# Kernel tuning notes

Hardware: AMD Instinct MI355X
Metric: run time of the kernel (lower is better)

## Reference

```python
import jax, jax.numpy as jnp
import numpy as np

D = 256; H = 8; L = 4; P = 4; DFF = 1024
B = 4; NQ = 900
SHAPES = np.array([[100, 160], [50, 80], [25, 40], [13, 20]], dtype=np.int64)
NV = int((SHAPES[:, 0] * SHAPES[:, 1]).sum())


def setup_inputs():
    key = jax.random.key(0)
    ks = jax.random.split(key, 16)
    def w(k, shape):
        return jax.random.normal(k, shape, jnp.float32) * 0.02
    return {
        "tgt": jax.random.normal(ks[0], (B, NQ, D), jnp.float32),
        "tgt_query_pos": jax.random.normal(ks[1], (B, NQ, D), jnp.float32),
        "tgt_reference_points": jax.random.uniform(ks[2], (B, NQ, L, 2), dtype=jnp.float32),
        "memory": jax.random.normal(ks[3], (B, NV, D), jnp.float32),
        "value_proj_w": w(ks[4], (D, D)), "value_proj_b": jnp.zeros((D,), jnp.float32),
        "samp_off_w": w(ks[5], (H * L * P * 2, D)), "samp_off_b": jnp.zeros((H * L * P * 2,), jnp.float32),
        "attn_w_w": w(ks[6], (H * L * P, D)), "attn_w_b": jnp.zeros((H * L * P,), jnp.float32),
        "ca_out_w": w(ks[7], (D, D)), "ca_out_b": jnp.zeros((D,), jnp.float32),
        "ln1_g": jnp.ones((D,), jnp.float32), "ln1_b": jnp.zeros((D,), jnp.float32),
        "in_proj_w": w(ks[8], (3 * D, D)), "in_proj_b": jnp.zeros((3 * D,), jnp.float32),
        "sa_out_w": w(ks[9], (D, D)), "sa_out_b": jnp.zeros((D,), jnp.float32),
        "ln2_g": jnp.ones((D,), jnp.float32), "ln2_b": jnp.zeros((D,), jnp.float32),
        "ffn1_w": w(ks[10], (DFF, D)), "ffn1_b": jnp.zeros((DFF,), jnp.float32),
        "ffn2_w": w(ks[11], (D, DFF)), "ffn2_b": jnp.zeros((D,), jnp.float32),
        "ln3_g": jnp.ones((D,), jnp.float32), "ln3_b": jnp.zeros((D,), jnp.float32),
        "spatial_shapes": jnp.asarray(SHAPES),
    }


def layer_norm(x, g, b, eps=1e-5):
    m = x.mean(-1, keepdims=True)
    v = ((x - m) ** 2).mean(-1, keepdims=True)
    return (x - m) / jnp.sqrt(v + eps) * g + b


def ms_deform_attn(query, refp, value, shapes, Wv, bv, Wo, bo, Wa, ba, Wout, bout):
    # query [B,Nq,D], refp [B,Nq,L,2] in [0,1], value [B,NV,D]; shapes: np [L,2] (H,W)
    Bq, Nq, Dm = query.shape
    dh = Dm // H
    v = (value @ Wv.T + bv).reshape(Bq, -1, H, dh)
    off = (query @ Wo.T + bo).reshape(Bq, Nq, H, L, P, 2)
    aw = jax.nn.softmax((query @ Wa.T + ba).reshape(Bq, Nq, H, L * P), axis=-1)
    aw = aw.reshape(Bq, Nq, H, L, P)
    norm = jnp.asarray(np.stack([shapes[:, 1], shapes[:, 0]], -1), jnp.float32)  # [L,2] = (W,H)
    loc = refp[:, :, None, :, None, :] + off / norm[None, None, None, :, None, :]  # [B,Nq,H,L,P,2]
    starts = np.concatenate([[0], np.cumsum(shapes[:, 0] * shapes[:, 1])])
    acc = jnp.zeros((Bq, Nq, H, dh), query.dtype)
    for l in range(L):
        Hl, Wl = int(shapes[l, 0]), int(shapes[l, 1])
        vf = v[:, int(starts[l]):int(starts[l]) + Hl * Wl]                 # [B,HW,H,dh]
        v2 = vf.transpose(0, 2, 1, 3).reshape(Bq * H, Hl * Wl, dh)
        # grid_sample align_corners=False: pixel = loc*size - 0.5
        xl = loc[:, :, :, l, :, 0] * Wl - 0.5                              # [B,Nq,H,P]
        yl = loc[:, :, :, l, :, 1] * Hl - 0.5
        x0 = jnp.floor(xl); y0 = jnp.floor(yl)
        wx = xl - x0; wy = yl - y0
        x0i = x0.astype(jnp.int32); y0i = y0.astype(jnp.int32)
        def corner(xi, yi, wgt):
            valid = (xi >= 0) & (xi < Wl) & (yi >= 0) & (yi < Hl)
            idx = jnp.clip(yi, 0, Hl - 1) * Wl + jnp.clip(xi, 0, Wl - 1)   # [B,Nq,H,P]
            idx2 = idx.transpose(0, 2, 1, 3).reshape(Bq * H, Nq * P)
            g = jnp.take_along_axis(v2, idx2[..., None], axis=1)           # [B*H,Nq*P,dh]
            g = g.reshape(Bq, H, Nq, P, dh).transpose(0, 2, 1, 3, 4)
            return g * (wgt * valid).astype(query.dtype)[..., None]
        s = (corner(x0i, y0i, (1 - wx) * (1 - wy))
             + corner(x0i + 1, y0i, wx * (1 - wy))
             + corner(x0i, y0i + 1, (1 - wx) * wy)
             + corner(x0i + 1, y0i + 1, wx * wy))                          # [B,Nq,H,P,dh]
        acc = acc + jnp.einsum('bqhpd,bqhp->bqhd', s, aw[:, :, :, l])
    return acc.reshape(Bq, Nq, Dm) @ Wout.T + bout


def mha(q, k, v, Win, bin_, Wout, bout):
    Dm = q.shape[-1]; dh = Dm // H
    def proj(x, W, b):
        return (x @ W.T + b).reshape(x.shape[0], x.shape[1], H, dh)
    qh = proj(q, Win[:Dm], bin_[:Dm])
    kh = proj(k, Win[Dm:2 * Dm], bin_[Dm:2 * Dm])
    vh = proj(v, Win[2 * Dm:], bin_[2 * Dm:])
    att = jax.nn.softmax(jnp.einsum('bqhd,bkhd->bhqk', qh, kh) / np.sqrt(dh).astype(np.float32), axis=-1)
    o = jnp.einsum('bhqk,bkhd->bqhd', att, vh).reshape(q.shape[0], q.shape[1], Dm)
    return o @ Wout.T + bout


def _forward(tgt, tgt_query_pos, tgt_reference_points, memory,
             value_proj_w, value_proj_b, samp_off_w, samp_off_b, attn_w_w, attn_w_b,
             ca_out_w, ca_out_b, ln1_g, ln1_b, in_proj_w, in_proj_b, sa_out_w, sa_out_b,
             ln2_g, ln2_b, ffn1_w, ffn1_b, ffn2_w, ffn2_b, ln3_g, ln3_b, shapes):
    # cross (deformable) attention
    q = tgt + tgt_query_pos
    tgt2 = ms_deform_attn(q, tgt_reference_points, memory, shapes,
                          value_proj_w, value_proj_b, samp_off_w, samp_off_b,
                          attn_w_w, attn_w_b, ca_out_w, ca_out_b)
    x = layer_norm(tgt + tgt2, ln1_g, ln1_b)
    # self attention (q=k=x+pos, v=x)
    qk = x + tgt_query_pos
    x = layer_norm(x + mha(qk, qk, x, in_proj_w, in_proj_b, sa_out_w, sa_out_b), ln2_g, ln2_b)
    # FFN
    ff = jax.nn.relu(x @ ffn1_w.T + ffn1_b) @ ffn2_w.T + ffn2_b
    return layer_norm(x + ff, ln3_g, ln3_b)


def reference(tgt, tgt_query_pos, tgt_reference_points, memory,
              value_proj_w, value_proj_b, samp_off_w, samp_off_b, attn_w_w, attn_w_b,
              ca_out_w, ca_out_b, ln1_g, ln1_b, in_proj_w, in_proj_b, sa_out_w, sa_out_b,
              ln2_g, ln2_b, ffn1_w, ffn1_b, ffn2_w, ffn2_b, ln3_g, ln3_b, spatial_shapes):
    shapes = np.asarray(spatial_shapes)
    return _forward(tgt, tgt_query_pos, tgt_reference_points, memory,
                    value_proj_w, value_proj_b, samp_off_w, samp_off_b, attn_w_w, attn_w_b,
                    ca_out_w, ca_out_b, ln1_g, ln1_b, in_proj_w, in_proj_b, sa_out_w, sa_out_b,
                    ln2_g, ln2_b, ffn1_w, ffn1_b, ffn2_w, ffn2_b, ln3_g, ln3_b, shapes)
```

## Files before the change

kernel.cpp:

```cpp
#include <hip/hip_runtime.h>

constexpr int D_   = 256;
constexpr int H_   = 8;
constexpr int DH   = 32;
constexpr int L_   = 4;
constexpr int P_   = 4;
constexpr int DFF_ = 1024;
constexpr int B_   = 4;
constexpr int NQ_  = 900;
constexpr int NV_  = 21260;
constexpr int MQ   = B_ * NQ_;
constexpr int MV   = B_ * NV_;

typedef __attribute__((ext_vector_type(8))) short short8;
typedef __attribute__((ext_vector_type(4))) float f32x4;

static __device__ __forceinline__ unsigned short f2bf(float x) {
  union { float f; unsigned int u; } v;
  v.f = x;
  const unsigned int r = v.u + 0x7fffu + ((v.u >> 16) & 1u);
  return (unsigned short)(r >> 16);
}
static __device__ __forceinline__ float bf2f(unsigned short u) {
  union { unsigned int i; float f; } x;
  x.i = ((unsigned int)u) << 16;
  return x.f;
}

struct CvtArgs {
  const float* src[9];
  unsigned short* dst[9];
  int n[9];
  float scl[9];
};

__global__ __launch_bounds__(256) void cvtw(CvtArgs a) {
  const int seg = blockIdx.y;
  const int n = a.n[seg];
  const float s = a.scl[seg];
  const float* __restrict__ sp = a.src[seg];
  unsigned short* __restrict__ d = a.dst[seg];
  for (int i = (blockIdx.x * 256 + threadIdx.x) * 4; i < n;
       i += gridDim.x * 256 * 4) {
    const float4 v = *reinterpret_cast<const float4*>(&sp[i]);
    d[i + 0] = f2bf(v.x * s); d[i + 1] = f2bf(v.y * s);
    d[i + 2] = f2bf(v.z * s); d[i + 3] = f2bf(v.w * s);
  }
}

__global__ void biasprep(const float* __restrict__ bin,
                         const float* __restrict__ bo,
                         const float* __restrict__ ba,
                         float* __restrict__ bqk, float* __restrict__ bfu) {
  const int i = threadIdx.x;
  if (i < 512) bqk[i] = (i < 256) ? bin[i] * 0.17677669529663687f : bin[i];
  if (i < 384) bfu[i] = (i < 256) ? bo[i] : ba[i - 256];
}

template <int K, bool ABF, bool ADD2, bool RELU, bool OUTBF>
__global__ __launch_bounds__(256) void gemm_p2(
    const void* __restrict__ Ap, const float* __restrict__ A2,
    const unsigned short* __restrict__ Wbf, const float* __restrict__ bias,
    void* __restrict__ Cp, int M, int N) {
  constexpr int LDR = 40;
  constexpr int NT = K / 32;
  __shared__ unsigned short As[2][128][LDR];
  __shared__ unsigned short Bs[2][128][LDR];

  const float* Af = (const float*)Ap;
  const unsigned short* Ab = (const unsigned short*)Ap;
  float* Cf = (float*)Cp;
  unsigned short* Cb = (unsigned short*)Cp;

  const int t    = threadIdx.x;
  const int wave = t >> 6;
  const int l    = t & 63;
  const int n0   = blockIdx.x * 128;
  const int m0   = blockIdx.y * 128;
  const int wm   = (wave >> 1) * 64;
  const int wn   = (wave & 1) * 64;
  const int srow = t >> 1;
  const int sseg = (t & 1) * 16;
  const int lr   = l & 15;
  const int lk   = (l >> 4) * 8;

  const int am = m0 + srow;
  const bool aok = am < M;
  const size_t arow = (size_t)am * K;
  const size_t brow = (size_t)(n0 + srow) * K;

  f32x4 acc[4][4];
#pragma unroll
  for (int i = 0; i < 4; ++i)
#pragma unroll
    for (int j = 0; j < 4; ++j) acc[i][j] = (f32x4)0.f;

  float  frA[16], frB[16];
  short8 abA0, abA1, abB0, abB1;
  short8 brA0, brA1, brB0, brB1;

#define LOAD_SLOT(SUF, k0)                                                     \
  do {                                                                         \
    if constexpr (ABF) {                                                       \
      if (aok) {                                                               \
        ab##SUF##0 = *reinterpret_cast<const short8*>(&Ab[arow + (k0) + sseg]);\
        ab##SUF##1 = *reinterpret_cast<const short8*>(&Ab[arow + (k0) + sseg + 8]);\
      } else {                                                                 \
        ab##SUF##0 = (short8)(short)0; ab##SUF##1 = (short8)(short)0;          \
      }                                                                        \
    } else {                                                                   \
      if (aok) {                                                               \
        _Pragma("unroll")                                                      \
        for (int j = 0; j < 4; ++j) {                                          \
          const float4 av =                                                    \
              *reinterpret_cast<const float4*>(&Af[arow + (k0) + sseg + 4 * j]);\
          fr##SUF[4 * j + 0] = av.x; fr##SUF[4 * j + 1] = av.y;                \
          fr##SUF[4 * j + 2] = av.z; fr##SUF[4 * j + 3] = av.w;                \
        }                                                                      \
        if constexpr (ADD2) {                                                  \
          _Pragma("unroll")                                                    \
          for (int j = 0; j < 4; ++j) {                                        \
            const float4 av =                                                  \
                *reinterpret_cast<const float4*>(&A2[arow + (k0) + sseg + 4 * j]);\
            fr##SUF[4 * j + 0] += av.x; fr##SUF[4 * j + 1] += av.y;            \
            fr##SUF[4 * j + 2] += av.z; fr##SUF[4 * j + 3] += av.w;            \
          }                                                                    \
        }                                                                      \
      } else {                                                                 \
        _Pragma("unroll")                                                      \
        for (int j = 0; j < 16; ++j) fr##SUF[j] = 0.f;                         \
      }                                                                        \
    }                                                                          \
    br##SUF##0 = *reinterpret_cast<const short8*>(&Wbf[brow + (k0) + sseg]);   \
    br##SUF##1 = *reinterpret_cast<const short8*>(&Wbf[brow + (k0) + sseg + 8]);\
  } while (0)

#define WRITE_SLOT(SUF, BUF)                                                   \
  do {                                                                         \
    if constexpr (ABF) {                                                       \
      *reinterpret_cast<short8*>(&As[BUF][srow][sseg])     = ab##SUF##0;       \
      *reinterpret_cast<short8*>(&As[BUF][srow][sseg + 8]) = ab##SUF##1;       \
    } else {                                                                   \
      alignas(16) unsigned short u[16];                                        \
      _Pragma("unroll")                                                        \
      for (int j = 0; j < 16; ++j) u[j] = f2bf(fr##SUF[j]);                    \
      *reinterpret_cast<short8*>(&As[BUF][srow][sseg]) =                       \
          *reinterpret_cast<short8*>(&u[0]);                                   \
      *reinterpret_cast<short8*>(&As[BUF][srow][sseg + 8]) =                   \
          *reinterpret_cast<short8*>(&u[8]);                                   \
    }                                                                          \
    *reinterpret_cast<short8*>(&Bs[BUF][srow][sseg])     = br##SUF##0;         \
    *reinterpret_cast<short8*>(&Bs[BUF][srow][sseg + 8]) = br##SUF##1;         \
  } while (0)

#define MFMA_STEP(BUF)                                                         \
  do {                                                                         \
    short8 af0 = *reinterpret_cast<const short8*>(&As[BUF][wm +  0 + lr][lk]); \
    short8 af1 = *reinterpret_cast<const short8*>(&As[BUF][wm + 16 + lr][lk]); \
    short8 af2 = *reinterpret_cast<const short8*>(&As[BUF][wm + 32 + lr][lk]); \
    short8 af3 = *reinterpret_cast<const short8*>(&As[BUF][wm + 48 + lr][lk]); \
    short8 bf0 = *reinterpret_cast<const short8*>(&Bs[BUF][wn +  0 + lr][lk]); \
    short8 bf1 = *reinterpret_cast<const short8*>(&Bs[BUF][wn + 16 + lr][lk]); \
    short8 bf2 = *reinterpret_cast<const short8*>(&Bs[BUF][wn + 32 + lr][lk]); \
    short8 bf3 = *reinterpret_cast<const short8*>(&Bs[BUF][wn + 48 + lr][lk]); \
    acc[0][0] = __builtin_amdgcn_mfma_f32_16x16x32_bf16(af0, bf0, acc[0][0], 0, 0, 0); \
    acc[0][1] = __builtin_amdgcn_mfma_f32_16x16x32_bf16(af0, bf1, acc[0][1], 0, 0, 0); \
    acc[0][2] = __builtin_amdgcn_mfma_f32_16x16x32_bf16(af0, bf2, acc[0][2], 0, 0, 0); \
    acc[0][3] = __builtin_amdgcn_mfma_f32_16x16x32_bf16(af0, bf3, acc[0][3], 0, 0, 0); \
    acc[1][0] = __builtin_amdgcn_mfma_f32_16x16x32_bf16(af1, bf0, acc[1][0], 0, 0, 0); \
    acc[1][1] = __builtin_amdgcn_mfma_f32_16x16x32_bf16(af1, bf1, acc[1][1], 0, 0, 0); \
    acc[1][2] = __builtin_amdgcn_mfma_f32_16x16x32_bf16(af1, bf2, acc[1][2], 0, 0, 0); \
    acc[1][3] = __builtin_amdgcn_mfma_f32_16x16x32_bf16(af1, bf3, acc[1][3], 0, 0, 0); \
    acc[2][0] = __builtin_amdgcn_mfma_f32_16x16x32_bf16(af2, bf0, acc[2][0], 0, 0, 0); \
    acc[2][1] = __builtin_amdgcn_mfma_f32_16x16x32_bf16(af2, bf1, acc[2][1], 0, 0, 0); \
    acc[2][2] = __builtin_amdgcn_mfma_f32_16x16x32_bf16(af2, bf2, acc[2][2], 0, 0, 0); \
    acc[2][3] = __builtin_amdgcn_mfma_f32_16x16x32_bf16(af2, bf3, acc[2][3], 0, 0, 0); \
    acc[3][0] = __builtin_amdgcn_mfma_f32_16x16x32_bf16(af3, bf0, acc[3][0], 0, 0, 0); \
    acc[3][1] = __builtin_amdgcn_mfma_f32_16x16x32_bf16(af3, bf1, acc[3][1], 0, 0, 0); \
    acc[3][2] = __builtin_amdgcn_mfma_f32_16x16x32_bf16(af3, bf2, acc[3][2], 0, 0, 0); \
    acc[3][3] = __builtin_amdgcn_mfma_f32_16x16x32_bf16(af3, bf3, acc[3][3], 0, 0, 0); \
  } while (0)

  LOAD_SLOT(A, 0);
  LOAD_SLOT(B, 32);
#pragma unroll
  for (int tt = 0; tt < NT; tt += 2) {
    WRITE_SLOT(A, 0);
    if (tt + 2 < NT) LOAD_SLOT(A, (tt + 2) * 32);
    __syncthreads();
    MFMA_STEP(0);

    WRITE_SLOT(B, 1);
    if (tt + 3 < NT) LOAD_SLOT(B, (tt + 3) * 32);
    __syncthreads();
    MFMA_STEP(1);
  }
#undef LOAD_SLOT
#undef WRITE_SLOT
#undef MFMA_STEP

  const int orow = (l >> 4) * 4;
#pragma unroll
  for (int fi = 0; fi < 4; ++fi) {
#pragma unroll
    for (int fj = 0; fj < 4; ++fj) {
      const int n = n0 + wn + fj * 16 + lr;
      const float bn = bias[n];
#pragma unroll
      for (int i = 0; i < 4; ++i) {
        const int m = m0 + wm + fi * 16 + orow + i;
        if (m < M) {
          float vv = acc[fi][fj][i] + bn;
          if (RELU) vv = fmaxf(vv, 0.f);
          if (OUTBF)
            Cb[(size_t)m * N + n] = f2bf(vv);
          else
            Cf[(size_t)m * N + n] = vv;
        }
      }
    }
  }
}

template <bool ABF, bool ADD2, bool RELU, bool OUTBF>
__global__ __launch_bounds__(256) void gemm_bres(
    const void* __restrict__ Ap, const float* __restrict__ A2,
    const unsigned short* __restrict__ Wbf, const float* __restrict__ bias,
    void* __restrict__ Cp, int M, int N) {
  __shared__ unsigned short Bs[32768];
  __shared__ unsigned short As[2][64][40];

  const float* Af = (const float*)Ap;
  const unsigned short* Ab = (const unsigned short*)Ap;
  float* Cf = (float*)Cp;
  unsigned short* Cb = (unsigned short*)Cp;

  const int t    = threadIdx.x;
  const int wave = t >> 6;
  const int l    = t & 63;
  const int n0   = blockIdx.x * 128;
  const int m0   = blockIdx.y * 64;
  const int wm   = (wave >> 1) * 32;
  const int wcg  = (wave & 1) * 4;
  const int lr   = l & 15;
  const int lk8  = (l >> 4) * 8;

#pragma unroll
  for (int i = 0; i < 16; ++i) {
    const int e  = i * 256 + t;
    const int el = e & 63;
    const int cg = (e >> 6) & 7;
    const int st = e >> 9;
    const int row = n0 + cg * 16 + (el & 15);
    const int col = st * 32 + ((el >> 4) * 8);
    *reinterpret_cast<short8*>(&Bs[e * 8]) =
        *reinterpret_cast<const short8*>(&Wbf[(size_t)row * 256 + col]);
  }

  const int arow = t >> 2;
  const int acol = (t & 3) * 8;
  const int am   = m0 + arow;
  const bool aok = am < M;
  const size_t abase = (size_t)am * 256 + acol;

  float  fr[3][8];
  short8 br_[3];

  auto ALOAD = [&](int slot, int tt) {
    const int k0 = tt * 32;
    if constexpr (ABF) {
      br_[slot] = aok ? *reinterpret_cast<const short8*>(&Ab[abase + k0])
                      : (short8)(short)0;
    } else {
      if (aok) {
        const float4 a0 = *reinterpret_cast<const float4*>(&Af[abase + k0]);
        const float4 a1 = *reinterpret_cast<const float4*>(&Af[abase + k0 + 4]);
        fr[slot][0] = a0.x; fr[slot][1] = a0.y;
        fr[slot][2] = a0.z; fr[slot][3] = a0.w;
        fr[slot][4] = a1.x; fr[slot][5] = a1.y;
        fr[slot][6] = a1.z; fr[slot][7] = a1.w;
        if constexpr (ADD2) {
          const float4 b0 = *reinterpret_cast<const float4*>(&A2[abase + k0]);
          const float4 b1 = *reinterpret_cast<const float4*>(&A2[abase + k0 + 4]);
          fr[slot][0] += b0.x; fr[slot][1] += b0.y;
          fr[slot][2] += b0.z; fr[slot][3] += b0.w;
          fr[slot][4] += b1.x; fr[slot][5] += b1.y;
          fr[slot][6] += b1.z; fr[slot][7] += b1.w;
        }
      } else {
#pragma unroll
        for (int j = 0; j < 8; ++j) fr[slot][j] = 0.f;
      }
    }
  };
  auto AWRITE = [&](int slot, int tt) {
    if constexpr (ABF) {
      *reinterpret_cast<short8*>(&As[tt & 1][arow][acol]) = br_[slot];
    } else {
      alignas(16) unsigned short u[8];
#pragma unroll
      for (int j = 0; j < 8; ++j) u[j] = f2bf(fr[slot][j]);
      *reinterpret_cast<short8*>(&As[tt & 1][arow][acol]) =
          *reinterpret_cast<short8*>(&u[0]);
    }
  };

  f32x4 acc[2][4];
#pragma unroll
  for (int fi = 0; fi < 2; ++fi)
#pragma unroll
    for (int fj = 0; fj < 4; ++fj) acc[fi][fj] = (f32x4)0.f;

  ALOAD(0, 0); ALOAD(1, 1); ALOAD(2, 2);

#pragma unroll
  for (int tt = 0; tt < 8; ++tt) {
    AWRITE(tt % 3, tt);
    if (tt + 3 < 8) ALOAD(tt % 3, tt + 3);
    __syncthreads();

    short8 afr[2];
#pragma unroll
    for (int fi = 0; fi < 2; ++fi)
      afr[fi] = *reinterpret_cast<const short8*>(&As[tt & 1][wm + fi * 16 + lr][lk8]);

#pragma unroll
    for (int fj = 0; fj < 4; ++fj) {
      const short8 bfr = *reinterpret_cast<const short8*>(
          &Bs[(((tt * 8) + wcg + fj) * 64 + l) * 8]);
      acc[0][fj] = __builtin_amdgcn_mfma_f32_16x16x32_bf16(afr[0], bfr, acc[0][fj], 0, 0, 0);
      acc[1][fj] = __builtin_amdgcn_mfma_f32_16x16x32_bf16(afr[1], bfr, acc[1][fj], 0, 0, 0);
    }
  }

  const int or4 = (l >> 4) * 4;
#pragma unroll
  for (int fi = 0; fi < 2; ++fi) {
#pragma unroll
    for (int fj = 0; fj < 4; ++fj) {
      const int n = n0 + (wave & 1) * 64 + fj * 16 + lr;
      const float bn = bias[n];
#pragma unroll
      for (int i = 0; i < 4; ++i) {
        const int m = m0 + wm + fi * 16 + or4 + i;
        if (m < M) {
          float vv = acc[fi][fj][i] + bn;
          if (RELU) vv = fmaxf(vv, 0.f);
          if (OUTBF)
            Cb[(size_t)m * N + n] = f2bf(vv);
          else
            Cf[(size_t)m * N + n] = vv;
        }
      }
    }
  }
}

__global__ __launch_bounds__(256) void deform(const float* __restrict__ refp,
                                              const float* __restrict__ offlog,
                                              const unsigned short* __restrict__ v,
                                              float* __restrict__ acc) {
  __shared__ float aw[H_ * L_ * P_];
  const int bq = blockIdx.x;
  const int b  = bq / NQ_;
  const int t  = threadIdx.x;
  const int h  = t >> 5, d = t & 31;

  if (t < 128) aw[t] = offlog[(size_t)bq * 384 + 256 + t];
  __syncthreads();
  if (t < 8) {
    float mx = -1e30f;
#pragma unroll
    for (int i = 0; i < 16; ++i) mx = fmaxf(mx, aw[t * 16 + i]);
    float e[16], s = 0.f;
#pragma unroll
    for (int i = 0; i < 16; ++i) { e[i] = expf(aw[t * 16 + i] - mx); s += e[i]; }
    const float inv = 1.f / s;
#pragma unroll
    for (int i = 0; i < 16; ++i) aw[t * 16 + i] = e[i] * inv;
  }
  __syncthreads();

  constexpr int ST[4] = {0, 16000, 20000, 21000};
  constexpr int HL[4] = {100, 50, 25, 13};
  constexpr int WL[4] = {160, 80, 40, 20};

  float a = 0.f;
#pragma unroll
  for (int l = 0; l < L_; ++l) {
    const float rx = refp[(bq * L_ + l) * 2 + 0];
    const float ry = refp[(bq * L_ + l) * 2 + 1];
    const float Wf = (float)WL[l], Hf = (float)HL[l];
    const int   Wi = WL[l], Hi = HL[l];
    const int vbase = (b * NV_ + ST[l]) * D_ + h * DH + d;
#pragma unroll
    for (int p = 0; p < P_; ++p) {
      const float ox = offlog[(size_t)bq * 384 + h * 32 + l * 8 + p * 2 + 0];
      const float oy = offlog[(size_t)bq * 384 + h * 32 + l * 8 + p * 2 + 1];
      const float locx = rx + ox / Wf;
      const float locy = ry + oy / Hf;
      const float xl = locx * Wf - 0.5f;
      const float yl = locy * Hf - 0.5f;
      const float x0 = floorf(xl), y0 = floorf(yl);
      const float wx = xl - x0, wy = yl - y0;
      const int x0i = (int)x0, y0i = (int)y0;
      const float w = aw[h * 16 + l * 4 + p];

      float s = 0.f;
#pragma unroll
      for (int c = 0; c < 4; ++c) {
        const int xi = x0i + (c & 1);
        const int yi = y0i + (c >> 1);
        const float cw = ((c & 1) ? wx : 1.f - wx) * ((c >> 1) ? wy : 1.f - wy);
        const bool valid = (xi >= 0) && (xi < Wi) && (yi >= 0) && (yi < Hi);
        const int xc = min(max(xi, 0), Wi - 1);
        const int yc = min(max(yi, 0), Hi - 1);
        const float g = bf2f(v[vbase + (yc * Wi + xc) * D_]);
        s += valid ? g * cw : 0.f;
      }
      a += w * s;
    }
  }
  acc[bq * D_ + t] = a;
}

constexpr int TQM  = 64;
constexpr int NQTM = (NQ_ + TQM - 1) / TQM;

__global__ __launch_bounds__(256) void mha_mfma(
    const unsigned short* __restrict__ qkh,
    const unsigned short* __restrict__ vh,
    unsigned short* __restrict__ o) {
  __shared__ unsigned short Qs[64][40];
  __shared__ unsigned short Ks[64][40];
  __shared__ unsigned short Vts[32][72];
  __shared__ unsigned short Ps[64][72];

  const int bx = blockIdx.x;
  const int qt = bx % NQTM;
  const int h  = (bx / NQTM) % H_;
  const int b  = bx / (NQTM * H_);
  const int t  = threadIdx.x;
  const int wave = t >> 6;
  const int l    = t & 63;
  const int q0   = qt * TQM;
  const int wrow = wave * 16;
  const int lr   = l & 15;
  const int lkb  = (l >> 4) * 8;

  {
    const int r = t >> 2, cb = (t & 3) * 8;
    short8 u;
    if (q0 + r < NQ_)
      u = *reinterpret_cast<const short8*>(
          &qkh[(size_t)(b * NQ_ + q0 + r) * 512 + h * DH + cb]);
    else
      u = (short8)(short)0;
    *reinterpret_cast<short8*>(&Qs[r][cb]) = u;
  }
  __syncthreads();

  const short8 qa = *reinterpret_cast<const short8*>(&Qs[wrow + lr][lkb]);

  f32x4 oacc[2];
  oacc[0] = (f32x4)0.f; oacc[1] = (f32x4)0.f;
  float m_[4] = {-1e30f, -1e30f, -1e30f, -1e30f};
  float l_[4] = {0.f, 0.f, 0.f, 0.f};

  for (int kt = 0; kt < NQTM; ++kt) {
    const int k0 = kt * 64;
    const int nk = min(64, NQ_ - k0);
    __syncthreads();

    {
      const int r = t >> 2, cb = (t & 3) * 8;
      short8 u;
      if (r < nk)
        u = *reinterpret_cast<const short8*>(
            &qkh[(size_t)(b * NQ_ + k0 + r) * 512 + 256 + h * DH + cb]);
      else
        u = (short8)(short)0;
      *reinterpret_cast<short8*>(&Ks[r][cb]) = u;
    }
    {
      const int k = t & 63, db = (t >> 6) * 8;
      short8 u;
      if (k < nk)
        u = *reinterpret_cast<const short8*>(
            &vh[(size_t)(b * NQ_ + k0 + k) * D_ + h * DH + db]);
      else
        u = (short8)(short)0;
#pragma unroll
      for (int j = 0; j < 8; ++j) Vts[db + j][k] = (unsigned short)u[j];
    }
    __syncthreads();

    f32x4 sacc[4];
#pragma unroll
    for (int fj = 0; fj < 4; ++fj)
      sacc[fj] = __builtin_amdgcn_mfma_f32_16x16x32_bf16(
          qa, *reinterpret_cast<const short8*>(&Ks[16 * fj + lr][lkb]),
          (f32x4)0.f, 0, 0, 0);

    bool cv[4];
#pragma unroll
    for (int fj = 0; fj < 4; ++fj) cv[fj] = (16 * fj + lr) < nk;

    float p0[4], p1[4], p2[4], p3[4], sc_[4];
#pragma unroll
    for (int i = 0; i < 4; ++i) {
      float tm = -1e30f;
      if (cv[0]) tm = fmaxf(tm, sacc[0][i]);
      if (cv[1]) tm = fmaxf(tm, sacc[1][i]);
      if (cv[2]) tm = fmaxf(tm, sacc[2][i]);
      if (cv[3]) tm = fmaxf(tm, sacc[3][i]);
      tm = fmaxf(tm, __shfl_xor(tm, 1));
      tm = fmaxf(tm, __shfl_xor(tm, 2));
      tm = fmaxf(tm, __shfl_xor(tm, 4));
      tm = fmaxf(tm, __shfl_xor(tm, 8));
      const float mn = fmaxf(m_[i], tm);
      sc_[i] = __expf(m_[i] - mn);
      m_[i] = mn;
      const float e0 = cv[0] ? __expf(sacc[0][i] - mn) : 0.f;
      const float e1 = cv[1] ? __expf(sacc[1][i] - mn) : 0.f;
      const float e2 = cv[2] ? __expf(sacc[2][i] - mn) : 0.f;
      const float e3 = cv[3] ? __expf(sacc[3][i] - mn) : 0.f;
      p0[i] = e0; p1[i] = e1; p2[i] = e2; p3[i] = e3;
      float rs = e0 + e1 + e2 + e3;
      rs += __shfl_xor(rs, 1);
      rs += __shfl_xor(rs, 2);
      rs += __shfl_xor(rs, 4);
      rs += __shfl_xor(rs, 8);
      l_[i] = l_[i] * sc_[i] + rs;
    }

#pragma unroll
    for (int i = 0; i < 4; ++i) {
      const int pr = wrow + (l >> 4) * 4 + i;
      Ps[pr][0  + lr] = f2bf(p0[i]);
      Ps[pr][16 + lr] = f2bf(p1[i]);
      Ps[pr][32 + lr] = f2bf(p2[i]);
      Ps[pr][48 + lr] = f2bf(p3[i]);
    }
    __syncthreads();

    const short8 pa0 = *reinterpret_cast<const short8*>(&Ps[wrow + lr][lkb]);
    const short8 pa1 = *reinterpret_cast<const short8*>(&Ps[wrow + lr][lkb + 32]);
#pragma unroll
    for (int nt = 0; nt < 2; ++nt) {
      f32x4 c = oacc[nt];
#pragma unroll
      for (int i = 0; i < 4; ++i) c[i] *= sc_[i];
      c = __builtin_amdgcn_mfma_f32_16x16x32_bf16(
          pa0, *reinterpret_cast<const short8*>(&Vts[16 * nt + lr][lkb]), c, 0, 0, 0);
      c = __builtin_amdgcn_mfma_f32_16x16x32_bf16(
          pa1, *reinterpret_cast<const short8*>(&Vts[16 * nt + lr][lkb + 32]), c, 0, 0, 0);
      oacc[nt] = c;
    }
  }

#pragma unroll
  for (int i = 0; i < 4; ++i) {
    const int r = (l >> 4) * 4 + i;
    const int q = q0 + wrow + r;
    if (q < NQ_) {
      const float inv = 1.f / l_[i];
      o[(size_t)(b * NQ_ + q) * D_ + h * DH + 0  + lr] = f2bf(oacc[0][i] * inv);
      o[(size_t)(b * NQ_ + q) * D_ + h * DH + 16 + lr] = f2bf(oacc[1][i] * inv);
    }
  }
}

__global__ __launch_bounds__(256) void ln(const float* __restrict__ res,
                                          const float* __restrict__ add,
                                          const float* __restrict__ g,
                                          const float* __restrict__ bt,
                                          float* __restrict__ out) {
  __shared__ float red[256];
  const int r = blockIdx.x, t = threadIdx.x;
  const float x = res[r * D_ + t] + add[r * D_ + t];
  red[t] = x;
  __syncthreads();
  for (int s = 128; s > 0; s >>= 1) {
    if (t < s) red[t] += red[t + s];
    __syncthreads();
  }
  const float mean = red[0] * (1.f / D_);
  __syncthreads();
  const float dx = x - mean;
  red[t] = dx * dx;
  __syncthreads();
  for (int s = 128; s > 0; s >>= 1) {
    if (t < s) red[t] += red[t + s];
    __syncthreads();
  }
  const float var = red[0] * (1.f / D_);
  out[r * D_ + t] = dx * rsqrtf(var + 1e-5f) * g[t] + bt[t];
}

extern "C" void kernel_launch(void* const* d_in, const int* in_sizes, int n_in,
                              void* d_out, int out_size, void* d_ws,
                              size_t ws_size, hipStream_t stream) {
  const float* tgt   = (const float*)d_in[0];
  const float* pos   = (const float*)d_in[1];
  const float* refp  = (const float*)d_in[2];
  const float* mem   = (const float*)d_in[3];
  const float* Wv    = (const float*)d_in[4];
  const float* bv    = (const float*)d_in[5];
  const float* Wo    = (const float*)d_in[6];
  const float* bo    = (const float*)d_in[7];
  const float* Wa    = (const float*)d_in[8];
  const float* ba    = (const float*)d_in[9];
  const float* Wca   = (const float*)d_in[10];
  const float* bca   = (const float*)d_in[11];
  const float* g1    = (const float*)d_in[12];
  const float* b1    = (const float*)d_in[13];
  const float* Win   = (const float*)d_in[14];
  const float* bin   = (const float*)d_in[15];
  const float* Wsa   = (const float*)d_in[16];
  const float* bsa   = (const float*)d_in[17];
  const float* g2    = (const float*)d_in[18];
  const float* b2    = (const float*)d_in[19];
  const float* W1    = (const float*)d_in[20];
  const float* bb1   = (const float*)d_in[21];
  const float* W2    = (const float*)d_in[22];
  const float* bb2   = (const float*)d_in[23];
  const float* g3    = (const float*)d_in[24];
  const float* b3    = (const float*)d_in[25];

  char* cur = (char*)d_ws;
  auto alloc = [&](size_t bytes) {
    char* p = cur;
    cur += (bytes + 255) & ~(size_t)255;
    return (void*)p;
  };
  unsigned short* v_bf    = (unsigned short*)alloc((size_t)MV * 256 * 2);
  float*          offlog  = (float*)alloc((size_t)MQ * 384 * 4);
  float*          accb    = (float*)alloc((size_t)MQ * 256 * 4);
  float*          tmp     = (float*)alloc((size_t)MQ * 256 * 4);
  float*          x1      = (float*)alloc((size_t)MQ * 256 * 4);
  float*          x2      = (float*)alloc((size_t)MQ * 256 * 4);
  unsigned short* qkh_bf  = (unsigned short*)alloc((size_t)MQ * 512 * 2);
  unsigned short* vh_bf   = (unsigned short*)alloc((size_t)MQ * 256 * 2);
  unsigned short* obuf_bf = (unsigned short*)alloc((size_t)MQ * 256 * 2);
  unsigned short* h1_bf   = (unsigned short*)alloc((size_t)MQ * 1024 * 2);
  unsigned short* Wv_bf   = (unsigned short*)alloc(65536 * 2);
  unsigned short* Wfu_bf  = (unsigned short*)alloc(98304 * 2);
  unsigned short* Wca_bf  = (unsigned short*)alloc(65536 * 2);
  unsigned short* Win_bf  = (unsigned short*)alloc(196608 * 2);
  unsigned short* Wsa_bf  = (unsigned short*)alloc(65536 * 2);
  unsigned short* W1_bf   = (unsigned short*)alloc(262144 * 2);
  unsigned short* W2_bf   = (unsigned short*)alloc(262144 * 2);
  float*          biasqk  = (float*)alloc(512 * 4);
  float*          bfused  = (float*)alloc(384 * 4);

  const float qscale = 0.17677669529663687f;

  CvtArgs ca;
  ca.src[0] = Wv;            ca.dst[0] = Wv_bf;          ca.n[0] = 65536;  ca.scl[0] = 1.f;
  ca.src[1] = Wo;            ca.dst[1] = Wfu_bf;         ca.n[1] = 65536;  ca.scl[1] = 1.f;
  ca.src[2] = Wa;            ca.dst[2] = Wfu_bf + 65536; ca.n[2] = 32768;  ca.scl[2] = 1.f;
  ca.src[3] = Wca;           ca.dst[3] = Wca_bf;         ca.n[3] = 65536;  ca.scl[3] = 1.f;
  ca.src[4] = Win;           ca.dst[4] = Win_bf;         ca.n[4] = 65536;  ca.scl[4] = qscale;
  ca.src[5] = Win + 65536;   ca.dst[5] = Win_bf + 65536; ca.n[5] = 131072; ca.scl[5] = 1.f;
  ca.src[6] = Wsa;           ca.dst[6] = Wsa_bf;         ca.n[6] = 65536;  ca.scl[6] = 1.f;
  ca.src[7] = W1;            ca.dst[7] = W1_bf;          ca.n[7] = 262144; ca.scl[7] = 1.f;
  ca.src[8] = W2;            ca.dst[8] = W2_bf;          ca.n[8] = 262144; ca.scl[8] = 1.f;
  cvtw<<<dim3(64, 9), 256, 0, stream>>>(ca);
  biasprep<<<1, 512, 0, stream>>>(bin, bo, ba, biasqk, bfused);

  const int mqb64  = (MQ + 63) / 64;
  const int mvb128 = (MV + 127) / 128;

  gemm_p2<256, false, false, false, true><<<dim3(2, mvb128), 256, 0, stream>>>(
      mem, nullptr, Wv_bf, bv, v_bf, MV, 256);
  gemm_bres<false, true, false, false><<<dim3(3, mqb64), 256, 0, stream>>>(
      tgt, pos, Wfu_bf, bfused, offlog, MQ, 384);
  deform<<<MQ, 256, 0, stream>>>(refp, offlog, v_bf, accb);
  gemm_bres<false, false, false, false><<<dim3(2, mqb64), 256, 0, stream>>>(
      accb, nullptr, Wca_bf, bca, tmp, MQ, 256);
  ln<<<MQ, 256, 0, stream>>>(tgt, tmp, g1, b1, x1);
  gemm_bres<false, true, false, true><<<dim3(4, mqb64), 256, 0, stream>>>(
      x1, pos, Win_bf, biasqk, qkh_bf, MQ, 512);
  gemm_bres<false, false, false, true><<<dim3(2, mqb64), 256, 0, stream>>>(
      x1, nullptr, Win_bf + 512 * 256, bin + 512, vh_bf, MQ, 256);
  mha_mfma<<<B_ * H_ * NQTM, 256, 0, stream>>>(qkh_bf, vh_bf, obuf_bf);
  gemm_bres<true, false, false, false><<<dim3(2, mqb64), 256, 0, stream>>>(
      obuf_bf, nullptr, Wsa_bf, bsa, tmp, MQ, 256);
  ln<<<MQ, 256, 0, stream>>>(x1, tmp, g2, b2, x2);
  gemm_bres<false, false, true, true><<<dim3(8, mqb64), 256, 0, stream>>>(
      x2, nullptr, W1_bf, bb1, h1_bf, MQ, 1024);
  gemm_p2<1024, true, false, false, false><<<dim3(2, (MQ + 127) / 128), 256, 0, stream>>>(
      h1_bf, nullptr, W2_bf, bb2, tmp, MQ, 256);
  ln<<<MQ, 256, 0, stream>>>(x2, tmp, g3, b3, (float*)d_out);
}
```

Baseline: 237.7 us.

## Add dedicated value-projection GEMM keeping weight strip resident in LDS

```diff
diff --git a/kernel.cpp b/kernel.cpp
--- a/kernel.cpp
+++ b/kernel.cpp
@@ -55,6 +55,132 @@
   const int i = threadIdx.x;
   if (i < 512) bqk[i] = (i < 256) ? bin[i] * 0.17677669529663687f : bin[i];
   if (i < 384) bfu[i] = (i < 256) ? bo[i] : ba[i - 256];
+}
+
+__global__ __launch_bounds__(256) void gemm_vp(
+    const float* __restrict__ A, const unsigned short* __restrict__ Wbf,
+    const float* __restrict__ bias, unsigned short* __restrict__ C, int M) {
+  __shared__ unsigned short Bs[16384];
+  __shared__ unsigned short As[2][128][40];
+
+  const int t     = threadIdx.x;
+  const int wave  = t >> 6;
+  const int l     = t & 63;
+  const int n0    = blockIdx.x * 64;
+  const int mbase = blockIdx.y * 512;
+  const int wm    = (wave >> 1) * 64;
+  const int wnc   = (wave & 1);
+  const int lr    = l & 15;
+  const int lk    = (l >> 4) * 8;
+  const int srow  = t >> 1;
+  const int sseg  = (t & 1) * 16;
+
+#pragma unroll
+  for (int i = 0; i < 8; ++i) {
+    const int e  = i * 256 + t;
+    const int el = e & 63;
+    const int cg = (e >> 6) & 3;
+    const int st = e >> 8;
+    const int row = n0 + cg * 16 + (el & 15);
+    const int col = st * 32 + (el >> 4) * 8;
+    *reinterpret_cast<short8*>(&Bs[e * 8]) =
+        *reinterpret_cast<const short8*>(&Wbf[(size_t)row * 256 + col]);
+  }
+
+  f32x4 acc[4][2];
+#pragma unroll
+  for (int fi = 0; fi < 4; ++fi)
+#pragma unroll
+    for (int fj = 0; fj < 2; ++fj) acc[fi][fj] = (f32x4)0.f;
+
+  float frA[16], frB[16];
+
+#define VLOAD(SUF, s)                                                          \
+  do {                                                                         \
+    const int am_ = mbase + ((s) >> 3) * 128 + srow;                           \
+    const int k0_ = ((s) & 7) * 32;                                            \
+    if (am_ < M) {                                                             \
+      const size_t base_ = (size_t)am_ * 256 + k0_ + sseg;                     \
+      _Pragma("unroll")                                                        \
+      for (int j = 0; j < 4; ++j) {                                            \
+        const float4 av = *reinterpret_cast<const float4*>(&A[base_ + 4 * j]); \
+        fr##SUF[4 * j + 0] = av.x; fr##SUF[4 * j + 1] = av.y;                  \
+        fr##SUF[4 * j + 2] = av.z; fr##SUF[4 * j + 3] = av.w;                  \
+      }                                                                        \
+    } else {                                                                   \
+      _Pragma("unroll")                                                        \
+      for (int j = 0; j < 16; ++j) fr##SUF[j] = 0.f;                           \
+    }                                                                          \
+  } while (0)
+
+#define VWRITE(SUF, BUF)                                                       \
+  do {                                                                         \
+    alignas(16) unsigned short u[16];                                          \
+    _Pragma("unroll")                                                          \
+    for (int j = 0; j < 16; ++j) u[j] = f2bf(fr##SUF[j]);                      \
+    *reinterpret_cast<short8*>(&As[BUF][srow][sseg]) =                         \
+        *reinterpret_cast<short8*>(&u[0]);                                     \
+    *reinterpret_cast<short8*>(&As[BUF][srow][sseg + 8]) =                     \
+        *reinterpret_cast<short8*>(&u[8]);                                     \
+  } while (0)
+
+#define VMFMA(s, BUF)                                                          \
+  do {                                                                         \
+    short8 af0 = *reinterpret_cast<const short8*>(&As[BUF][wm +  0 + lr][lk]); \
+    short8 af1 = *reinterpret_cast<const short8*>(&As[BUF][wm + 16 + lr][lk]); \
+    short8 af2 = *reinterpret_cast<const short8*>(&As[BUF][wm + 32 + lr][lk]); \
+    short8 af3 = *reinterpret_cast<const short8*>(&As[BUF][wm + 48 + lr][lk]); \
+    short8 bf0 = *reinterpret_cast<const short8*>(                             \
+        &Bs[((((s) & 7) * 4 + wnc * 2 + 0) * 64 + l) * 8]);                    \
+    short8 bf1 = *reinterpret_cast<const short8*>(                             \
+        &Bs[((((s) & 7) * 4 + wnc * 2 + 1) * 64 + l) * 8]);                    \
+    acc[0][0] = __builtin_amdgcn_mfma_f32_16x16x32_bf16(af0, bf0, acc[0][0], 0, 0, 0); \
+    acc[0][1] = __builtin_amdgcn_mfma_f32_16x16x32_bf16(af0, bf1, acc[0][1], 0, 0, 0); \
+    acc[1][0] = __builtin_amdgcn_mfma_f32_16x16x32_bf16(af1, bf0, acc[1][0], 0, 0, 0); \
+    acc[1][1] = __builtin_amdgcn_mfma_f32_16x16x32_bf16(af1, bf1, acc[1][1], 0, 0, 0); \
+    acc[2][0] = __builtin_amdgcn_mfma_f32_16x16x32_bf16(af2, bf0, acc[2][0], 0, 0, 0); \
+    acc[2][1] = __builtin_amdgcn_mfma_f32_16x16x32_bf16(af2, bf1, acc[2][1], 0, 0, 0); \
+    acc[3][0] = __builtin_amdgcn_mfma_f32_16x16x32_bf16(af3, bf0, acc[3][0], 0, 0, 0); \
+    acc[3][1] = __builtin_amdgcn_mfma_f32_16x16x32_bf16(af3, bf1, acc[3][1], 0, 0, 0); \
+  } while (0)
+
+#define VEPI(pt)                                                               \
+  do {                                                                         \
+    _Pragma("unroll")                                                          \
+    for (int fi = 0; fi < 4; ++fi) {                                           \
+      _Pragma("unroll")                                                        \
+      for (int fj = 0; fj < 2; ++fj) {                                         \
+        const int n_ = n0 + wnc * 32 + fj * 16 + lr;                           \
+        const float bn_ = bias[n_];                                            \
+        _Pragma("unroll")                                                      \
+        for (int i = 0; i < 4; ++i) {                                          \
+          const int m_ = mbase + (pt) * 128 + wm + fi * 16 + (l >> 4) * 4 + i; \
+          if (m_ < M) C[(size_t)m_ * 256 + n_] = f2bf(acc[fi][fj][i] + bn_);   \
+        }                                                                      \
+        acc[fi][fj] = (f32x4)0.f;                                              \
+      }                                                                        \
+    }                                                                          \
+  } while (0)
+
+  VLOAD(A, 0);
+  VLOAD(B, 1);
+#pragma unroll
+  for (int s = 0; s < 32; s += 2) {
+    VWRITE(A, 0);
+    if (s + 2 < 32) VLOAD(A, s + 2);
+    __syncthreads();
+    VMFMA(s, 0);
+
+    VWRITE(B, 1);
+    if (s + 3 < 32) VLOAD(B, s + 3);
+    __syncthreads();
+    VMFMA(s + 1, 1);
+    if (((s + 1) & 7) == 7) VEPI((s + 1) >> 3);
+  }
+#undef VLOAD
+#undef VWRITE
+#undef VMFMA
+#undef VEPI
 }
 
 template <int K, bool ABF, bool ADD2, bool RELU, bool OUTBF>
@@ -669,11 +795,10 @@
   cvtw<<<dim3(64, 9), 256, 0, stream>>>(ca);
   biasprep<<<1, 512, 0, stream>>>(bin, bo, ba, biasqk, bfused);
 
-  const int mqb64  = (MQ + 63) / 64;
-  const int mvb128 = (MV + 127) / 128;
-
-  gemm_p2<256, false, false, false, true><<<dim3(2, mvb128), 256, 0, stream>>>(
-      mem, nullptr, Wv_bf, bv, v_bf, MV, 256);
+  const int mqb64 = (MQ + 63) / 64;
+
+  gemm_vp<<<dim3(4, (MV + 511) / 512), 256, 0, stream>>>(
+      mem, Wv_bf, bv, v_bf, MV);
   gemm_bres<false, true, false, false><<<dim3(3, mqb64), 256, 0, stream>>>(
       tgt, pos, Wfu_bf, bfused, offlog, MQ, 384);
   deform<<<MQ, 256, 0, stream>>>(refp, offlog, v_bf, accb);
```

Result: slower. 249.4 us, median of 2 (+5.0%).
